# Kernel optimization log

Measured on AMD Instinct MI355X. Metric: run time of the kernel, lower is better.

Reference implementation:

```python
import jax, jax.numpy as jnp
import numpy as np

NEG_POS_RATIO = 3
THETA = 0.01
NUM_CLASSES = 21
B, P = 64, 16320
POS_FRAC = 0.02


def setup_inputs() -> dict:
    key = jax.random.key(0)
    k1, k2, k3, k4, k5, k6 = jax.random.split(key, 6)
    loc_data = jax.random.normal(k1, (B, P, 4), dtype=jnp.float32)
    conf_data = jax.random.normal(k2, (B, P, NUM_CLASSES), dtype=jnp.float32)
    arm_conf_data = jax.random.normal(k3, (B, P, 2), dtype=jnp.float32)
    loc_t = jax.random.normal(k4, (B, P, 4), dtype=jnp.float32)
    labels = jax.random.randint(k5, (B, P), 1, NUM_CLASSES)
    is_pos = jax.random.uniform(k6, (B, P)) < POS_FRAC
    conf_t = jnp.where(is_pos, labels, 0).astype(jnp.int64)
    return {"loc_data": loc_data, "conf_data": conf_data,
            "arm_conf_data": arm_conf_data, "loc_t": loc_t, "conf_t": conf_t}


def _multibox_loss(loc_data, conf_data, arm_conf_data, loc_t, conf_t):
    num_priors = conf_t.shape[1]
    # ODM: zero out positives whose ARM objectness score P(obj) <= theta
    p_obj = jax.nn.softmax(arm_conf_data, axis=-1)[:, :, 1]          # [B,P]
    pos = (conf_t > 0) & (p_obj > THETA)                             # [B,P]

    # localization loss: smooth L1 over positive anchors (masked sum == masked gather + sum)
    diff = loc_data - loc_t
    ad = jnp.abs(diff)
    sl1 = jnp.where(ad < 1.0, 0.5 * ad * ad, ad - 0.5)               # [B,P,4]
    loss_l = jnp.sum(sl1 * pos[..., None].astype(sl1.dtype))

    # per-anchor CE loss: logsumexp(c) - c[target]
    lse = jax.nn.logsumexp(conf_data, axis=-1)                       # [B,P]
    true_logit = jnp.take_along_axis(conf_data, conf_t[..., None], axis=-1)[..., 0]
    loss_c_all = lse - true_logit                                    # [B,P]

    # hard negative mining: rank non-positive anchors by loss (double argsort)
    loss_for_rank = jnp.where(pos, 0.0, loss_c_all)
    rank = jnp.argsort(jnp.argsort(-loss_for_rank, axis=1), axis=1)  # [B,P]
    num_pos = jnp.sum(pos.astype(jnp.int32), axis=1, keepdims=True)  # [B,1]
    num_neg = jnp.minimum(NEG_POS_RATIO * num_pos, num_priors - 1)
    neg = rank < num_neg                                             # [B,P]

    sel = pos | neg
    loss_c = jnp.sum(jnp.where(sel, loss_c_all, 0.0))

    N = jnp.sum(num_pos).astype(loss_l.dtype)
    return loss_l / N, loss_c / N


def reference(loc_data, conf_data, arm_conf_data, loc_t, conf_t):
    return _multibox_loss(loc_data, conf_data, arm_conf_data, loc_t, conf_t)
```

## Files before the change

### kernel.cpp

```cpp
#include <hip/hip_runtime.h>

#define NUM_P 16320
#define NUM_C 21
#define THETA 0.01f
#define WPR 255

__device__ __forceinline__ void load_tile(
    const float* __restrict__ conf, const int* __restrict__ conft,
    const float* __restrict__ arm, int t, int tid,
    float4 (&rr)[6], int& tc, float2& av)
{
    const int base = t * 256;
    const float4* conf4 = (const float4*)(conf + (size_t)base * NUM_C);
    #pragma unroll
    for (int it = 0; it < 6; ++it) {
        const int i = tid + it * 256;
        if (i < 1344) rr[it] = conf4[i];
    }
    tc = conft[base + tid];
    av = ((const float2*)arm)[base + tid];
}

__device__ __forceinline__ void process_tile(
    const float* __restrict__ loc, const float* __restrict__ loct,
    const float* __restrict__ conf, const int* __restrict__ conft,
    const float* __restrict__ arm,
    int* __restrict__ partial_n, float* __restrict__ rankvals,
    float* __restrict__ partial_l, float* __restrict__ partial_c,
    int t, int stride, int ntiles, int tid,
    float* tile, float* red_l, float* red_c,
    float4 (&rr)[6], int& tc, float2& av)
{
    const int lane = tid & 63, w = tid >> 6;
    const int tcl = tc;
    const float2 avl = av;

    __syncthreads();
    {
        float4* tile4 = (float4*)tile;
        #pragma unroll
        for (int it = 0; it < 6; ++it) {
            const int i = tid + it * 256;
            if (i < 1344) tile4[i] = rr[it];
        }
    }
    __syncthreads();

    const int tpre = t + 2 * stride;
    if (tpre < ntiles)
        load_tile(conf, conft, arm, tpre, tid, rr, tc, av);

    const int a = t * 256 + tid;
    float ll = 0.f, cep = 0.f;
    bool pos = false;
    {
        const float* cf = &tile[tid * NUM_C];
        float mx = cf[0];
        #pragma unroll
        for (int j = 1; j < NUM_C; ++j) mx = fmaxf(mx, cf[j]);
        float s = 0.f;
        #pragma unroll
        for (int j = 0; j < NUM_C; ++j) s += __expf(cf[j] - mx);
        const float ce = mx + __logf(s) - cf[tcl];

        const float am = fmaxf(avl.x, avl.y);
        const float e0 = __expf(avl.x - am), e1 = __expf(avl.y - am);
        const float p1 = e1 / (e0 + e1);
        pos = (tcl > 0) && (p1 > THETA);

        if (pos) {
            cep = ce;
            const float4 lv = ((const float4*)loc)[a];
            const float4 tv = ((const float4*)loct)[a];
            const float dx[4] = { lv.x - tv.x, lv.y - tv.y, lv.z - tv.z, lv.w - tv.w };
            #pragma unroll
            for (int j = 0; j < 4; ++j) {
                const float ad = fabsf(dx[j]);
                ll += (ad < 1.f) ? 0.5f * ad * ad : ad - 0.5f;
            }
        }
        rankvals[a] = pos ? 0.f : ce;
    }

    const unsigned long long pm = __ballot(pos);
    #pragma unroll
    for (int off = 32; off > 0; off >>= 1) {
        ll  += __shfl_down(ll, off, 64);
        cep += __shfl_down(cep, off, 64);
    }
    if (lane == 0) {
        red_l[w] = ll;
        red_c[w] = cep;
        partial_n[t * 4 + w] = (int)__popcll(pm);
    }
    __syncthreads();
    if (tid == 0) {
        partial_l[t] = red_l[0] + red_l[1] + red_l[2] + red_l[3];
        partial_c[t] = red_c[0] + red_c[1] + red_c[2] + red_c[3];
    }
}

__global__ __launch_bounds__(256, 4) void anchor_kernel(
    const float* __restrict__ loc, const float* __restrict__ conf,
    const float* __restrict__ arm, const float* __restrict__ loct,
    const int* __restrict__ conft,
    int* __restrict__ partial_n, float* __restrict__ rankvals,
    float* __restrict__ partial_l, float* __restrict__ partial_c,
    int ntiles)
{
    __shared__ float tile[256 * NUM_C];
    __shared__ float red_l[4], red_c[4];
    const int tid = threadIdx.x;
    const int stride = gridDim.x;

    int t = blockIdx.x;
    if (t >= ntiles) return;

    float4 rA[6]; int tcA; float2 avA;
    float4 rB[6]; int tcB; float2 avB;
    load_tile(conf, conft, arm, t, tid, rA, tcA, avA);
    if (t + stride < ntiles)
        load_tile(conf, conft, arm, t + stride, tid, rB, tcB, avB);

    while (true) {
        process_tile(loc, loct, conf, conft, arm, partial_n, rankvals,
                     partial_l, partial_c, t, stride, ntiles, tid,
                     tile, red_l, red_c, rA, tcA, avA);
        t += stride;
        if (t >= ntiles) break;
        process_tile(loc, loct, conf, conft, arm, partial_n, rankvals,
                     partial_l, partial_c, t, stride, ntiles, tid,
                     tile, red_l, red_c, rB, tcB, avB);
        t += stride;
        if (t >= ntiles) break;
    }
}

__global__ __launch_bounds__(1024) void select_kernel(
    const float* __restrict__ rankvals, const int* __restrict__ partial_n,
    const float* __restrict__ partial_l, const float* __restrict__ partial_c,
    float* __restrict__ acc,
    int ntiles, float* __restrict__ out)
{
    __shared__ int hist1[256];
    __shared__ int hist2[2048];
    __shared__ float wred[16], wsl[16], wsc[16];
    __shared__ int s_b1, s_kk1, s_t19, s_kk2, s_np;

    const int b = blockIdx.x, tid = threadIdx.x;
    const int lane = tid & 63, w = tid >> 6;

    const uint4* row4 = (const uint4*)(rankvals + (size_t)b * NUM_P);
    uint4 rr[4];
    #pragma unroll
    for (int it = 0; it < 4; ++it) {
        const int i = tid + it * 1024;
        rr[it] = (i < NUM_P / 4) ? row4[i] : make_uint4(0u, 0u, 0u, 0u);
    }
    int rn = (tid < WPR) ? partial_n[b * WPR + tid] : 0;

    float sl = 0.f, sc = 0.f;
    {
        const int slice = (ntiles + gridDim.x - 1) / gridDim.x;
        const int s0 = b * slice, s1 = min(s0 + slice, ntiles);
        for (int i = s0 + tid; i < s1; i += 1024) { sl += partial_l[i]; sc += partial_c[i]; }
    }

    if (tid == 0) s_np = 0;
    if (tid < 256) hist1[tid] = 0;
    hist2[tid] = 0; hist2[tid + 1024] = 0;
    __syncthreads();

    #pragma unroll
    for (int off = 32; off > 0; off >>= 1) {
        rn += __shfl_down(rn, off, 64);
        sl += __shfl_down(sl, off, 64);
        sc += __shfl_down(sc, off, 64);
    }
    if (lane == 0) {
        wsl[w] = sl; wsc[w] = sc;
        if (rn) atomicAdd(&s_np, rn);
    }
    __syncthreads();

    const int np = s_np;
    const int k = min(3 * np, NUM_P - 1);
    float tot = 0.f;

    if (k > 0) {
        #pragma unroll
        for (int it = 0; it < 4; ++it) {
            const unsigned ub[4] = { rr[it].x, rr[it].y, rr[it].z, rr[it].w };
            #pragma unroll
            for (int j = 0; j < 4; ++j) {
                const unsigned bin = ub[j] >> 24;
                unsigned long long alive = ~0ULL;
                while (alive) {
                    const int leader = __ffsll(alive) - 1;
                    const unsigned lb = __shfl(bin, leader, 64);
                    const unsigned long long mm = __ballot(bin == lb);
                    if (lane == leader) atomicAdd(&hist1[lb], (int)__popcll(mm));
                    alive &= ~mm;
                }
            }
        }
        __syncthreads();
        if (tid < 64) {
            const int j0 = tid * 4;
            const int h0 = hist1[j0], h1 = hist1[j0+1], h2 = hist1[j0+2], h3 = hist1[j0+3];
            int ssum = h0 + h1 + h2 + h3;
            #pragma unroll
            for (int d = 1; d < 64; d <<= 1) {
                const int tmp = __shfl_down(ssum, d, 64);
                if (lane + d < 64) ssum += tmp;
            }
            const int bse = ssum - (h0 + h1 + h2 + h3);
            int S[5];
            S[0] = ssum; S[4] = bse;
            S[3] = bse + h3; S[2] = S[3] + h2; S[1] = S[2] + h1;
            #pragma unroll
            for (int jj = 0; jj < 4; ++jj)
                if (S[jj] >= k && S[jj + 1] < k) { s_b1 = j0 + jj; s_kk1 = k - S[jj + 1]; }
        }
        __syncthreads();
        const unsigned B1 = (unsigned)s_b1;
        const int kk1 = s_kk1;

        #pragma unroll
        for (int it = 0; it < 4; ++it) {
            const unsigned ub[4] = { rr[it].x, rr[it].y, rr[it].z, rr[it].w };
            #pragma unroll
            for (int j = 0; j < 4; ++j)
                if ((ub[j] >> 24) == B1) atomicAdd(&hist2[(ub[j] >> 13) & 0x7FFu], 1);
        }
        __syncthreads();
        const int h0 = hist2[2 * tid], h1 = hist2[2 * tid + 1];
        int suf = h0 + h1;
        #pragma unroll
        for (int d = 1; d < 64; d <<= 1) {
            const int tmp = __shfl_down(suf, d, 64);
            if (lane + d < 64) suf += tmp;
        }
        if (lane == 0) hist1[w] = suf;
        __syncthreads();
        int woff = 0;
        for (int ww = w + 1; ww < 16; ++ww) woff += hist1[ww];
        const int S0 = suf + woff;
        const int S1 = S0 - h0;
        const int S2 = S1 - h1;
        if (S0 >= kk1 && S1 < kk1) { s_t19 = (s_b1 << 11) | (2 * tid);     s_kk2 = kk1 - S1; }
        if (S1 >= kk1 && S2 < kk1) { s_t19 = (s_b1 << 11) | (2 * tid + 1); s_kk2 = kk1 - S2; }
        __syncthreads();
        const unsigned t19 = (unsigned)s_t19;
        const int kk2 = s_kk2;
        const float vth = __uint_as_float(t19 << 13);

        float partial = 0.f;
        #pragma unroll
        for (int it = 0; it < 4; ++it) {
            const unsigned ub[4] = { rr[it].x, rr[it].y, rr[it].z, rr[it].w };
            #pragma unroll
            for (int j = 0; j < 4; ++j)
                if ((ub[j] >> 13) > t19) partial += __uint_as_float(ub[j]);
        }
        #pragma unroll
        for (int off = 32; off > 0; off >>= 1)
            partial += __shfl_down(partial, off, 64);
        if (lane == 0) wred[w] = partial;
        __syncthreads();
        if (tid == 0) {
            #pragma unroll
            for (int wv = 0; wv < 16; ++wv) tot += wred[wv];
            tot += (float)kk2 * vth;
        }
    }

    if (tid == 0) {
        float SL = 0.f, SC = 0.f;
        #pragma unroll
        for (int wv = 0; wv < 16; ++wv) { SL += wsl[wv]; SC += wsc[wv]; }
        int* acc_i = (int*)acc;
        atomicAdd(&acc[0], SL);
        atomicAdd(&acc[1], SC + tot);
        atomicAdd(&acc_i[2], np);
        __threadfence();
        const int prev = atomicAdd(&acc_i[3], 1);
        if (prev == (int)gridDim.x - 1) {
            __threadfence();
            const float L = atomicAdd(&acc[0], 0.f);
            const float C = atomicAdd(&acc[1], 0.f);
            const int   N = atomicAdd(&acc_i[2], 0);
            out[0] = L / (float)N;
            out[1] = C / (float)N;
        }
    }
}

extern "C" void kernel_launch(void* const* d_in, const int* in_sizes, int n_in,
                              void* d_out, int out_size, void* d_ws, size_t ws_size,
                              hipStream_t stream) {
    const float* loc  = (const float*)d_in[0];
    const float* conf = (const float*)d_in[1];
    const float* arm  = (const float*)d_in[2];
    const float* loct = (const float*)d_in[3];
    const int*  conft = (const int*)d_in[4];
    float* out = (float*)d_out;

    const int total  = in_sizes[4];
    const int Bn     = total / NUM_P;
    const int ntiles = total / 256;

    float* acc       = (float*)d_ws;
    float* partial_l = (float*)((char*)d_ws + 1024);
    float* partial_c = (float*)((char*)d_ws + 17408);
    int*   partial_n = (int*)((char*)d_ws + 33792);
    float* rankvals  = (float*)((char*)d_ws + 99328);

    hipMemsetAsync(d_ws, 0, 64, stream);

    const int grid = min(ntiles, 1024);
    hipLaunchKernelGGL(anchor_kernel, dim3(grid), dim3(256), 0, stream,
                       loc, conf, arm, loct, conft, partial_n, rankvals,
                       partial_l, partial_c, ntiles);
    hipLaunchKernelGGL(select_kernel, dim3(Bn), dim3(1024), 0, stream,
                       rankvals, partial_n, partial_l, partial_c, acc, ntiles, out);
}
```

Measured before the change: 205.8 us.

## Fuse per-anchor loss and hard-negative selection into one per-row kernel

Merges the anchor kernel and the select kernel into a single kernel with one 1024-thread block per batch row. Each block streams its row's conf data in 16 tiles through shared memory with register prefetch and keeps the CE bits in registers for the radix selection. This removes the rankvals and partial arrays written to global memory and one kernel launch. In exchange, only 64 blocks (one per batch row) run, using about 86KB of shared memory each, so most CUs sit idle and bandwidth is likely underused.

```diff
diff --git a/kernel.cpp b/kernel.cpp
--- a/kernel.cpp
+++ b/kernel.cpp
@@ -3,205 +3,137 @@
 #define NUM_P 16320
 #define NUM_C 21
 #define THETA 0.01f
-#define WPR 255
-
-__device__ __forceinline__ void load_tile(
-    const float* __restrict__ conf, const int* __restrict__ conft,
-    const float* __restrict__ arm, int t, int tid,
-    float4 (&rr)[6], int& tc, float2& av)
-{
-    const int base = t * 256;
-    const float4* conf4 = (const float4*)(conf + (size_t)base * NUM_C);
-    #pragma unroll
-    for (int it = 0; it < 6; ++it) {
-        const int i = tid + it * 256;
-        if (i < 1344) rr[it] = conf4[i];
-    }
-    tc = conft[base + tid];
-    av = ((const float2*)arm)[base + tid];
-}
-
-__device__ __forceinline__ void process_tile(
-    const float* __restrict__ loc, const float* __restrict__ loct,
-    const float* __restrict__ conf, const int* __restrict__ conft,
-    const float* __restrict__ arm,
-    int* __restrict__ partial_n, float* __restrict__ rankvals,
-    float* __restrict__ partial_l, float* __restrict__ partial_c,
-    int t, int stride, int ntiles, int tid,
-    float* tile, float* red_l, float* red_c,
-    float4 (&rr)[6], int& tc, float2& av)
-{
-    const int lane = tid & 63, w = tid >> 6;
-    const int tcl = tc;
-    const float2 avl = av;
-
-    __syncthreads();
-    {
-        float4* tile4 = (float4*)tile;
-        #pragma unroll
-        for (int it = 0; it < 6; ++it) {
-            const int i = tid + it * 256;
-            if (i < 1344) tile4[i] = rr[it];
-        }
-    }
-    __syncthreads();
-
-    const int tpre = t + 2 * stride;
-    if (tpre < ntiles)
-        load_tile(conf, conft, arm, tpre, tid, rr, tc, av);
-
-    const int a = t * 256 + tid;
-    float ll = 0.f, cep = 0.f;
-    bool pos = false;
-    {
-        const float* cf = &tile[tid * NUM_C];
-        float mx = cf[0];
-        #pragma unroll
-        for (int j = 1; j < NUM_C; ++j) mx = fmaxf(mx, cf[j]);
-        float s = 0.f;
-        #pragma unroll
-        for (int j = 0; j < NUM_C; ++j) s += __expf(cf[j] - mx);
-        const float ce = mx + __logf(s) - cf[tcl];
-
-        const float am = fmaxf(avl.x, avl.y);
-        const float e0 = __expf(avl.x - am), e1 = __expf(avl.y - am);
-        const float p1 = e1 / (e0 + e1);
-        pos = (tcl > 0) && (p1 > THETA);
-
-        if (pos) {
-            cep = ce;
-            const float4 lv = ((const float4*)loc)[a];
-            const float4 tv = ((const float4*)loct)[a];
-            const float dx[4] = { lv.x - tv.x, lv.y - tv.y, lv.z - tv.z, lv.w - tv.w };
-            #pragma unroll
-            for (int j = 0; j < 4; ++j) {
-                const float ad = fabsf(dx[j]);
-                ll += (ad < 1.f) ? 0.5f * ad * ad : ad - 0.5f;
-            }
-        }
-        rankvals[a] = pos ? 0.f : ce;
-    }
-
-    const unsigned long long pm = __ballot(pos);
-    #pragma unroll
-    for (int off = 32; off > 0; off >>= 1) {
-        ll  += __shfl_down(ll, off, 64);
-        cep += __shfl_down(cep, off, 64);
-    }
-    if (lane == 0) {
-        red_l[w] = ll;
-        red_c[w] = cep;
-        partial_n[t * 4 + w] = (int)__popcll(pm);
-    }
-    __syncthreads();
-    if (tid == 0) {
-        partial_l[t] = red_l[0] + red_l[1] + red_l[2] + red_l[3];
-        partial_c[t] = red_c[0] + red_c[1] + red_c[2] + red_c[3];
-    }
-}
-
-__global__ __launch_bounds__(256, 4) void anchor_kernel(
+#define NTILE 16
+
+__global__ __launch_bounds__(1024) void fused_kernel(
     const float* __restrict__ loc, const float* __restrict__ conf,
     const float* __restrict__ arm, const float* __restrict__ loct,
     const int* __restrict__ conft,
-    int* __restrict__ partial_n, float* __restrict__ rankvals,
-    float* __restrict__ partial_l, float* __restrict__ partial_c,
-    int ntiles)
+    float* __restrict__ acc,
+    float* __restrict__ out)
 {
-    __shared__ float tile[256 * NUM_C];
-    __shared__ float red_l[4], red_c[4];
-    const int tid = threadIdx.x;
-    const int stride = gridDim.x;
-
-    int t = blockIdx.x;
-    if (t >= ntiles) return;
-
-    float4 rA[6]; int tcA; float2 avA;
-    float4 rB[6]; int tcB; float2 avB;
-    load_tile(conf, conft, arm, t, tid, rA, tcA, avA);
-    if (t + stride < ntiles)
-        load_tile(conf, conft, arm, t + stride, tid, rB, tcB, avB);
-
-    while (true) {
-        process_tile(loc, loct, conf, conft, arm, partial_n, rankvals,
-                     partial_l, partial_c, t, stride, ntiles, tid,
-                     tile, red_l, red_c, rA, tcA, avA);
-        t += stride;
-        if (t >= ntiles) break;
-        process_tile(loc, loct, conf, conft, arm, partial_n, rankvals,
-                     partial_l, partial_c, t, stride, ntiles, tid,
-                     tile, red_l, red_c, rB, tcB, avB);
-        t += stride;
-        if (t >= ntiles) break;
-    }
-}
-
-__global__ __launch_bounds__(1024) void select_kernel(
-    const float* __restrict__ rankvals, const int* __restrict__ partial_n,
-    const float* __restrict__ partial_l, const float* __restrict__ partial_c,
-    float* __restrict__ acc,
-    int ntiles, float* __restrict__ out)
-{
+    __shared__ float tile[1024 * NUM_C];
     __shared__ int hist1[256];
     __shared__ int hist2[2048];
-    __shared__ float wred[16], wsl[16], wsc[16];
-    __shared__ int s_b1, s_kk1, s_t19, s_kk2, s_np;
-
-    const int b = blockIdx.x, tid = threadIdx.x;
+    __shared__ float wred[16], sll[16], scc[16];
+    __shared__ int sni[16];
+    __shared__ int s_b1, s_kk1, s_t19, s_kk2;
+
+    const int b = blockIdx.x;
+    const int tid = threadIdx.x;
     const int lane = tid & 63, w = tid >> 6;
-
-    const uint4* row4 = (const uint4*)(rankvals + (size_t)b * NUM_P);
-    uint4 rr[4];
+    const size_t rowbase = (size_t)b * NUM_P;
+
+    unsigned cebits[NTILE];
+    float ll = 0.f, cep = 0.f;
+    int cnt = 0;
+
+    float4 rr[6];
+    int tc = 0; float2 av = make_float2(0.f, 0.f);
+    {
+        const float4* conf4 = (const float4*)(conf + rowbase * NUM_C);
+        #pragma unroll
+        for (int k = 0; k < 6; ++k) {
+            const int i = tid + k * 1024;
+            if (i < 5376) rr[k] = conf4[i];
+        }
+        tc = conft[rowbase + tid];
+        av = ((const float2*)arm)[rowbase + tid];
+    }
+
     #pragma unroll
-    for (int it = 0; it < 4; ++it) {
-        const int i = tid + it * 1024;
-        rr[it] = (i < NUM_P / 4) ? row4[i] : make_uint4(0u, 0u, 0u, 0u);
-    }
-    int rn = (tid < WPR) ? partial_n[b * WPR + tid] : 0;
-
-    float sl = 0.f, sc = 0.f;
-    {
-        const int slice = (ntiles + gridDim.x - 1) / gridDim.x;
-        const int s0 = b * slice, s1 = min(s0 + slice, ntiles);
-        for (int i = s0 + tid; i < s1; i += 1024) { sl += partial_l[i]; sc += partial_c[i]; }
-    }
-
-    if (tid == 0) s_np = 0;
+    for (int it = 0; it < NTILE; ++it) {
+        const int tsize = (it < NTILE - 1) ? 1024 : 960;
+        const int nfl4  = tsize * NUM_C / 4;
+        {
+            float4* tile4 = (float4*)tile;
+            #pragma unroll
+            for (int k = 0; k < 6; ++k) {
+                const int i = tid + k * 1024;
+                if (i < nfl4) tile4[i] = rr[k];
+            }
+        }
+        const int tcl = tc; const float2 avl = av;
+        __syncthreads();
+
+        if (it + 1 < NTILE) {
+            const int nsize = (it + 1 < NTILE - 1) ? 1024 : 960;
+            const int nn4 = nsize * NUM_C / 4;
+            const size_t nb = rowbase + (size_t)(it + 1) * 1024;
+            const float4* conf4 = (const float4*)(conf + nb * NUM_C);
+            #pragma unroll
+            for (int k = 0; k < 6; ++k) {
+                const int i = tid + k * 1024;
+                if (i < nn4) rr[k] = conf4[i];
+            }
+            if (tid < nsize) {
+                tc = conft[nb + tid];
+                av = ((const float2*)arm)[nb + tid];
+            }
+        }
+
+        unsigned rb = 0u;
+        if (tid < tsize) {
+            const float* cf = &tile[tid * NUM_C];
+            float mx = cf[0];
+            #pragma unroll
+            for (int j = 1; j < NUM_C; ++j) mx = fmaxf(mx, cf[j]);
+            float s = 0.f;
+            #pragma unroll
+            for (int j = 0; j < NUM_C; ++j) s += __expf(cf[j] - mx);
+            const float ce = mx + __logf(s) - cf[tcl];
+
+            const float am = fmaxf(avl.x, avl.y);
+            const float e0 = __expf(avl.x - am), e1 = __expf(avl.y - am);
+            const bool pos = (tcl > 0) && (e1 / (e0 + e1) > THETA);
+
+            if (pos) {
+                ++cnt; cep += ce;
+                const size_t a = rowbase + (size_t)it * 1024 + tid;
+                const float4 lv = ((const float4*)loc)[a];
+                const float4 tv = ((const float4*)loct)[a];
+                const float dx[4] = { lv.x-tv.x, lv.y-tv.y, lv.z-tv.z, lv.w-tv.w };
+                #pragma unroll
+                for (int j = 0; j < 4; ++j) {
+                    const float ad = fabsf(dx[j]);
+                    ll += (ad < 1.f) ? 0.5f * ad * ad : ad - 0.5f;
+                }
+            } else {
+                rb = __float_as_uint(ce);
+            }
+        }
+        cebits[it] = rb;
+        __syncthreads();
+    }
+
+    #pragma unroll
+    for (int off = 32; off > 0; off >>= 1) {
+        cnt += __shfl_down(cnt, off, 64);
+        ll  += __shfl_down(ll, off, 64);
+        cep += __shfl_down(cep, off, 64);
+    }
+    if (lane == 0) { sni[w] = cnt; sll[w] = ll; scc[w] = cep; }
     if (tid < 256) hist1[tid] = 0;
     hist2[tid] = 0; hist2[tid + 1024] = 0;
     __syncthreads();
 
+    int np = 0;
     #pragma unroll
-    for (int off = 32; off > 0; off >>= 1) {
-        rn += __shfl_down(rn, off, 64);
-        sl += __shfl_down(sl, off, 64);
-        sc += __shfl_down(sc, off, 64);
-    }
-    if (lane == 0) {
-        wsl[w] = sl; wsc[w] = sc;
-        if (rn) atomicAdd(&s_np, rn);
-    }
-    __syncthreads();
-
-    const int np = s_np;
+    for (int i = 0; i < 16; ++i) np += sni[i];
     const int k = min(3 * np, NUM_P - 1);
     float tot = 0.f;
 
     if (k > 0) {
         #pragma unroll
-        for (int it = 0; it < 4; ++it) {
-            const unsigned ub[4] = { rr[it].x, rr[it].y, rr[it].z, rr[it].w };
-            #pragma unroll
-            for (int j = 0; j < 4; ++j) {
-                const unsigned bin = ub[j] >> 24;
-                unsigned long long alive = ~0ULL;
-                while (alive) {
-                    const int leader = __ffsll(alive) - 1;
-                    const unsigned lb = __shfl(bin, leader, 64);
-                    const unsigned long long mm = __ballot(bin == lb);
-                    if (lane == leader) atomicAdd(&hist1[lb], (int)__popcll(mm));
-                    alive &= ~mm;
-                }
+        for (int it = 0; it < NTILE; ++it) {
+            const unsigned bin = cebits[it] >> 24;
+            unsigned long long alive = ~0ULL;
+            while (alive) {
+                const int leader = __ffsll(alive) - 1;
+                const unsigned lb = __shfl(bin, leader, 64);
+                const unsigned long long mm = __ballot(bin == lb);
+                if (lane == leader) atomicAdd(&hist1[lb], (int)__popcll(mm));
+                alive &= ~mm;
             }
         }
         __syncthreads();
@@ -227,11 +159,9 @@
         const int kk1 = s_kk1;
 
         #pragma unroll
-        for (int it = 0; it < 4; ++it) {
-            const unsigned ub[4] = { rr[it].x, rr[it].y, rr[it].z, rr[it].w };
-            #pragma unroll
-            for (int j = 0; j < 4; ++j)
-                if ((ub[j] >> 24) == B1) atomicAdd(&hist2[(ub[j] >> 13) & 0x7FFu], 1);
+        for (int it = 0; it < NTILE; ++it) {
+            const unsigned u = cebits[it];
+            if ((u >> 24) == B1) atomicAdd(&hist2[(u >> 13) & 0x7FFu], 1);
         }
         __syncthreads();
         const int h0 = hist2[2 * tid], h1 = hist2[2 * tid + 1];
@@ -245,24 +175,17 @@
         __syncthreads();
         int woff = 0;
         for (int ww = w + 1; ww < 16; ++ww) woff += hist1[ww];
-        const int S0 = suf + woff;
-        const int S1 = S0 - h0;
-        const int S2 = S1 - h1;
-        if (S0 >= kk1 && S1 < kk1) { s_t19 = (s_b1 << 11) | (2 * tid);     s_kk2 = kk1 - S1; }
-        if (S1 >= kk1 && S2 < kk1) { s_t19 = (s_b1 << 11) | (2 * tid + 1); s_kk2 = kk1 - S2; }
+        const int S0 = suf + woff, S1 = S0 - h0, S2 = S1 - h1;
+        if (S0 >= kk1 && S1 < kk1) { s_t19 = ((int)B1 << 11) | (2 * tid);     s_kk2 = kk1 - S1; }
+        if (S1 >= kk1 && S2 < kk1) { s_t19 = ((int)B1 << 11) | (2 * tid + 1); s_kk2 = kk1 - S2; }
         __syncthreads();
         const unsigned t19 = (unsigned)s_t19;
-        const int kk2 = s_kk2;
         const float vth = __uint_as_float(t19 << 13);
 
         float partial = 0.f;
         #pragma unroll
-        for (int it = 0; it < 4; ++it) {
-            const unsigned ub[4] = { rr[it].x, rr[it].y, rr[it].z, rr[it].w };
-            #pragma unroll
-            for (int j = 0; j < 4; ++j)
-                if ((ub[j] >> 13) > t19) partial += __uint_as_float(ub[j]);
-        }
+        for (int it = 0; it < NTILE; ++it)
+            if ((cebits[it] >> 13) > t19) partial += __uint_as_float(cebits[it]);
         #pragma unroll
         for (int off = 32; off > 0; off >>= 1)
             partial += __shfl_down(partial, off, 64);
@@ -270,15 +193,15 @@
         __syncthreads();
         if (tid == 0) {
             #pragma unroll
-            for (int wv = 0; wv < 16; ++wv) tot += wred[wv];
-            tot += (float)kk2 * vth;
+            for (int i = 0; i < 16; ++i) tot += wred[i];
+            tot += (float)s_kk2 * vth;
         }
     }
 
     if (tid == 0) {
         float SL = 0.f, SC = 0.f;
         #pragma unroll
-        for (int wv = 0; wv < 16; ++wv) { SL += wsl[wv]; SC += wsc[wv]; }
+        for (int i = 0; i < 16; ++i) { SL += sll[i]; SC += scc[i]; }
         int* acc_i = (int*)acc;
         atomicAdd(&acc[0], SL);
         atomicAdd(&acc[1], SC + tot);
@@ -306,22 +229,12 @@
     const int*  conft = (const int*)d_in[4];
     float* out = (float*)d_out;
 
-    const int total  = in_sizes[4];
-    const int Bn     = total / NUM_P;
-    const int ntiles = total / 256;
-
-    float* acc       = (float*)d_ws;
-    float* partial_l = (float*)((char*)d_ws + 1024);
-    float* partial_c = (float*)((char*)d_ws + 17408);
-    int*   partial_n = (int*)((char*)d_ws + 33792);
-    float* rankvals  = (float*)((char*)d_ws + 99328);
-
+    const int total = in_sizes[4];
+    const int Bn = total / NUM_P;
+
+    float* acc = (float*)d_ws;
     hipMemsetAsync(d_ws, 0, 64, stream);
 
-    const int grid = min(ntiles, 1024);
-    hipLaunchKernelGGL(anchor_kernel, dim3(grid), dim3(256), 0, stream,
-                       loc, conf, arm, loct, conft, partial_n, rankvals,
-                       partial_l, partial_c, ntiles);
-    hipLaunchKernelGGL(select_kernel, dim3(Bn), dim3(1024), 0, stream,
-                       rankvals, partial_n, partial_l, partial_c, acc, ntiles, out);
+    hipLaunchKernelGGL(fused_kernel, dim3(Bn), dim3(1024), 0, stream,
+                       loc, conf, arm, loct, conft, acc, out);
 }
```

New measurement: 263.6 us. 28.1% more time.
